# Kernel optimization log

Hardware: AMD Instinct MI355X
Metric: run time of the kernel (lower is better)

Reference implementation:

```python
import jax, jax.numpy as jnp
import numpy as np

# Faithful JAX reference for MVLiftingModule.lift_2D_to_3D with lifting_method='mean'.
# Torch semantics: for each batch, view, and part p in [1, parts_nb[b]] (in order),
# scatter-write the (weighted softmax) pixel prediction into each point that any
# Since each pixel's predicted part is unique (argmax), the winning pixel per point
# is the one maximizing key = pred_class * H*W + flat_pixel_index. We compute that
# deterministically via scatter-max, then gather features and voint-mean over views.

def setup_inputs() -> dict:
    key = jax.random.key(0)
    k1, k2, k3, k4, k5 = jax.random.split(key, 5)
    B, N, V, C, H, W = 4, 2048, 12, 50, 128, 128
    points = jax.random.normal(k1, (B, N, 3), dtype=jnp.float32)
    predictions_2d = jax.random.normal(k2, (B, V, C, H, W), dtype=jnp.float32)
    # -1 marks background pixels (no point), as in pytorch3d pix_to_face
    rendered_pix_to_point = jax.random.randint(k3, (B, V, 1, H, W), -1, N, dtype=jnp.int32)
    views_weights = jax.random.uniform(k4, (B, V, 1, 1, 1), dtype=jnp.float32)
    parts_nb = jax.random.randint(k5, (B,), 1, 7, dtype=jnp.int32)
    return {"points": points, "predictions_2d": predictions_2d,
            "rendered_pix_to_point": rendered_pix_to_point,
            "views_weights": views_weights, "parts_nb": parts_nb}


def reference(points, predictions_2d, rendered_pix_to_point, views_weights, parts_nb):
    B, N, _ = points.shape
    _, V, C, H, W = predictions_2d.shape
    P = H * W

    p2p = rendered_pix_to_point[:, :, 0]            # (B,V,H,W)
    valid = p2p != -1                                # pix_to_face_mask
    idx = jnp.where(valid, p2p % N, 0)               # invalid pixels -> point 0 (as in torch)

    probs = jax.nn.softmax(predictions_2d, axis=2)   # softmax over classes
    pred_max = jnp.argmax(probs, axis=2).astype(jnp.int32)   # (B,V,H,W)
    feats = (views_weights * probs).reshape(B, V, C, P)       # weighted predictions

    # pixel participates iff valid and its predicted part in [1, parts_nb[b]]
    mask_pix = valid & (pred_max >= 1) & (pred_max <= parts_nb[:, None, None, None])
    mask_pix = mask_pix.reshape(B, V, P)
    idx_f = idx.reshape(B, V, P)

    pix = jnp.arange(P, dtype=jnp.int32)
    kkey = pred_max.reshape(B, V, P) * P + pix
    kkey = jnp.where(mask_pix, kkey, -1)

    bi = jnp.arange(B)[:, None, None]
    vi = jnp.arange(V)[None, :, None]
    winner = jnp.full((B, V, N), -1, dtype=jnp.int32).at[bi, vi, idx_f].max(kkey)

    voints_mask = (winner >= 0)                      # (B,V,N)
    win_pix = jnp.where(voints_mask, winner % P, 0)  # winning pixel per point/view

    # gather weighted features at winning pixel: (B,V,C,N)
    point_feats = jnp.take_along_axis(feats, win_pix[:, :, None, :], axis=3)
    m = voints_mask.astype(feats.dtype)
    masked = point_feats * m[:, :, None, :]

    # vointmean: masked mean over views -> (B,C,N)
    denom = jnp.maximum(m.sum(axis=1), 1.0)          # (B,N)
    labels_3d_feats = masked.sum(axis=1) / denom[:, None, :]
    return labels_3d_feats
```

## Files before the change

### kernel.cpp

```cpp
#include <hip/hip_runtime.h>

#define B 4
#define N 2048
#define V 12
#define C 50
#define P 16384

__global__ __launch_bounds__(256) void k1_argmax_scatter(
    const float4* __restrict__ predv,
    const int4*  __restrict__ p2pv,
    const int*   __restrict__ parts_nb,
    int*         __restrict__ winner,
    float4*      __restrict__ sexp) {
  const int PQ = P / 4;
  int t = blockIdx.x * 256 + threadIdx.x;
  if (t >= B * V * PQ) return;
  int q  = t % PQ;
  int bv = t / PQ;
  int b  = bv / V;

  size_t base = (size_t)bv * C * PQ + q;
  float4 x = predv[base];
  float m0 = x.x, m1 = x.y, m2 = x.z, m3 = x.w;
  float s0 = __expf(x.x), s1 = __expf(x.y), s2 = __expf(x.z), s3 = __expf(x.w);
  int   a0 = 0,  a1 = 0,  a2 = 0,  a3 = 0;
  for (int c = 1; c < C; ++c) {
    float4 y = predv[base + (size_t)c * PQ];
    if (y.x > m0) { m0 = y.x; a0 = c; }
    if (y.y > m1) { m1 = y.y; a1 = c; }
    if (y.z > m2) { m2 = y.z; a2 = c; }
    if (y.w > m3) { m3 = y.w; a3 = c; }
    s0 += __expf(y.x); s1 += __expf(y.y);
    s2 += __expf(y.z); s3 += __expf(y.w);
  }
  sexp[(size_t)bv * PQ + q] = make_float4(s0, s1, s2, s3);

  int4 pt = p2pv[(size_t)bv * PQ + q];
  int pn = parts_nb[b];
  int p0 = q * 4;
  int* wbase = winner + bv * N;
  if (pt.x != -1 && a0 >= 1 && a0 <= pn) atomicMax(wbase + pt.x, a0 * P + p0);
  if (pt.y != -1 && a1 >= 1 && a1 <= pn) atomicMax(wbase + pt.y, a1 * P + p0 + 1);
  if (pt.z != -1 && a2 >= 1 && a2 <= pn) atomicMax(wbase + pt.z, a2 * P + p0 + 2);
  if (pt.w != -1 && a3 >= 1 && a3 <= pn) atomicMax(wbase + pt.w, a3 * P + p0 + 3);
}

__global__ __launch_bounds__(256) void k2_gather(
    const float* __restrict__ pred,
    const int*   __restrict__ winner,
    const float* __restrict__ sexp,
    const float* __restrict__ vw,
    float*       __restrict__ out) {
  int wid  = blockIdx.x * (256 / 64) + (threadIdx.x >> 6);
  int lane = threadIdx.x & 63;
  int b = wid >> 11;
  int n = wid & (N - 1);

  int wv[V];
  #pragma unroll
  for (int v = 0; v < V; ++v) wv[v] = winner[(b * V + v) * N + n];

  float acc = 0.f;
  int cnt = 0;
  #pragma unroll
  for (int v = 0; v < V; ++v) {
    bool valid = wv[v] >= 0;
    int wp = valid ? (wv[v] & (P - 1)) : 0;
    size_t bvo = (size_t)(b * V + v);
    float l = (lane < C) ? pred[(bvo * C + lane) * P + wp] : 0.f;
    float s = sexp[bvo * P + wp];
    float w = vw[b * V + v] / s;
    cnt += valid ? 1 : 0;
    acc += valid ? __expf(l) * w : 0.f;
  }
  float denom = (float)(cnt > 0 ? cnt : 1);
  if (lane < C)
    out[((size_t)b * C + lane) * N + n] = acc / denom;
}

extern "C" void kernel_launch(void* const* d_in, const int* in_sizes, int n_in,
                              void* d_out, int out_size, void* d_ws, size_t ws_size,
                              hipStream_t stream) {
  const float* pred  = (const float*)d_in[1];
  const int*   p2p   = (const int*)d_in[2];
  const float* vw    = (const float*)d_in[3];
  const int*   parts = (const int*)d_in[4];
  float* out = (float*)d_out;

  int*   winner = (int*)d_ws;
  float* sexp   = (float*)((char*)d_ws + (size_t)B * V * N * sizeof(int));

  hipMemsetAsync(winner, 0xFF, (size_t)B * V * N * sizeof(int), stream);

  int nthreads1 = B * V * (P / 4);
  k1_argmax_scatter<<<(nthreads1 + 255) / 256, 256, 0, stream>>>(
      (const float4*)pred, (const int4*)p2p, parts, winner, (float4*)sexp);

  k2_gather<<<(B * N) / 4, 256, 0, stream>>>(pred, winner, sexp, vw, out);
}
```

Before: 270.3 us.

## Compute softmax only for winning pixels and stage features in point-major buffer

Removes the per-pixel exp-sum from the argmax/scatter pass so that pass only computes argmax. A new extract kernel finds each point's winning pixel, computes its softmax and view weighting, and writes all classes contiguously into a per-point buffer. The final reduction then reads coalesced rows instead of strided gathers from the prediction tensor. This adds a kernel launch and a second read of the prediction tensor for winning pixels, which are scattered reads with a strided per-class pattern.

```diff
diff --git a/kernel.cpp b/kernel.cpp
--- a/kernel.cpp
+++ b/kernel.cpp
@@ -5,13 +5,13 @@
 #define V 12
 #define C 50
 #define P 16384
+#define CP 64
 
 __global__ __launch_bounds__(256) void k1_argmax_scatter(
     const float4* __restrict__ predv,
     const int4*  __restrict__ p2pv,
     const int*   __restrict__ parts_nb,
-    int*         __restrict__ winner,
-    float4*      __restrict__ sexp) {
+    int*         __restrict__ winner) {
   const int PQ = P / 4;
   int t = blockIdx.x * 256 + threadIdx.x;
   if (t >= B * V * PQ) return;
@@ -22,7 +22,6 @@
   size_t base = (size_t)bv * C * PQ + q;
   float4 x = predv[base];
   float m0 = x.x, m1 = x.y, m2 = x.z, m3 = x.w;
-  float s0 = __expf(x.x), s1 = __expf(x.y), s2 = __expf(x.z), s3 = __expf(x.w);
   int   a0 = 0,  a1 = 0,  a2 = 0,  a3 = 0;
   for (int c = 1; c < C; ++c) {
     float4 y = predv[base + (size_t)c * PQ];
@@ -30,10 +29,7 @@
     if (y.y > m1) { m1 = y.y; a1 = c; }
     if (y.z > m2) { m2 = y.z; a2 = c; }
     if (y.w > m3) { m3 = y.w; a3 = c; }
-    s0 += __expf(y.x); s1 += __expf(y.y);
-    s2 += __expf(y.z); s3 += __expf(y.w);
   }
-  sexp[(size_t)bv * PQ + q] = make_float4(s0, s1, s2, s3);
 
   int4 pt = p2pv[(size_t)bv * PQ + q];
   int pn = parts_nb[b];
@@ -45,37 +41,61 @@
   if (pt.w != -1 && a3 >= 1 && a3 <= pn) atomicMax(wbase + pt.w, a3 * P + p0 + 3);
 }
 
-__global__ __launch_bounds__(256) void k2_gather(
+__global__ __launch_bounds__(256) void k1b_extract(
     const float* __restrict__ pred,
+    const int*   __restrict__ p2p,
     const int*   __restrict__ winner,
-    const float* __restrict__ sexp,
     const float* __restrict__ vw,
+    float*       __restrict__ wfeat) {
+  int t = blockIdx.x * 256 + threadIdx.x;
+  int p  = t & (P - 1);
+  int bv = t >> 14;
+
+  int pt = p2p[(size_t)bv * P + p];
+  if (pt == -1) return;
+  int bvn = bv * N + pt;
+  int key = winner[bvn];
+  if (key < 0 || (key & (P - 1)) != p) return;
+
+  const float* pp = pred + (size_t)bv * C * P + p;
+  float e[C];
+  float s = 0.f;
+  #pragma unroll
+  for (int c = 0; c < C; ++c) e[c] = pp[(size_t)c * P];
+  #pragma unroll
+  for (int c = 0; c < C; ++c) { e[c] = __expf(e[c]); s += e[c]; }
+  float w = vw[bv] / s;
+
+  float4* dst = (float4*)(wfeat + (size_t)bvn * CP);
+  #pragma unroll
+  for (int c4 = 0; c4 < C / 4; ++c4) {
+    dst[c4] = make_float4(e[4*c4] * w, e[4*c4+1] * w, e[4*c4+2] * w, e[4*c4+3] * w);
+  }
+  wfeat[(size_t)bvn * CP + 48] = e[48] * w;
+  wfeat[(size_t)bvn * CP + 49] = e[49] * w;
+}
+
+__global__ __launch_bounds__(256) void k3_reduce(
+    const int*   __restrict__ winner,
+    const float* __restrict__ wfeat,
     float*       __restrict__ out) {
-  int wid  = blockIdx.x * (256 / 64) + (threadIdx.x >> 6);
+  int wid  = blockIdx.x * 4 + (threadIdx.x >> 6);
   int lane = threadIdx.x & 63;
   int b = wid >> 11;
   int n = wid & (N - 1);
-
-  int wv[V];
-  #pragma unroll
-  for (int v = 0; v < V; ++v) wv[v] = winner[(b * V + v) * N + n];
 
   float acc = 0.f;
   int cnt = 0;
   #pragma unroll
   for (int v = 0; v < V; ++v) {
-    bool valid = wv[v] >= 0;
-    int wp = valid ? (wv[v] & (P - 1)) : 0;
-    size_t bvo = (size_t)(b * V + v);
-    float l = (lane < C) ? pred[(bvo * C + lane) * P + wp] : 0.f;
-    float s = sexp[bvo * P + wp];
-    float w = vw[b * V + v] / s;
+    int bvn = (b * V + v) * N + n;
+    bool valid = winner[bvn] >= 0;
+    float f = (valid && lane < C) ? wfeat[(size_t)bvn * CP + lane] : 0.f;
     cnt += valid ? 1 : 0;
-    acc += valid ? __expf(l) * w : 0.f;
+    acc += f;
   }
-  float denom = (float)(cnt > 0 ? cnt : 1);
   if (lane < C)
-    out[((size_t)b * C + lane) * N + n] = acc / denom;
+    out[((size_t)b * C + lane) * N + n] = acc / (float)(cnt > 0 ? cnt : 1);
 }
 
 extern "C" void kernel_launch(void* const* d_in, const int* in_sizes, int n_in,
@@ -88,13 +108,17 @@
   float* out = (float*)d_out;
 
   int*   winner = (int*)d_ws;
-  float* sexp   = (float*)((char*)d_ws + (size_t)B * V * N * sizeof(int));
+  float* wfeat  = (float*)((char*)d_ws + (size_t)B * V * N * sizeof(int));
 
   hipMemsetAsync(winner, 0xFF, (size_t)B * V * N * sizeof(int), stream);
 
   int nthreads1 = B * V * (P / 4);
   k1_argmax_scatter<<<(nthreads1 + 255) / 256, 256, 0, stream>>>(
-      (const float4*)pred, (const int4*)p2p, parts, winner, (float4*)sexp);
+      (const float4*)pred, (const int4*)p2p, parts, winner);
 
-  k2_gather<<<(B * N) / 4, 256, 0, stream>>>(pred, winner, sexp, vw, out);
+  int nthreads1b = B * V * P;
+  k1b_extract<<<nthreads1b / 256, 256, 0, stream>>>(
+      pred, p2p, winner, vw, wfeat);
+
+  k3_reduce<<<(B * N) / 4, 256, 0, stream>>>(winner, wfeat, out);
 }
```

After: 259.8 us. -3.9%, faster.

## Compact winning-candidate softmax rows into a pool to avoid scattered prediction gathers

Applied to the files above, without the earlier changes.

Each pixel that passes the part mask now takes a slot from a global atomic counter. It writes its 50 exponentiated logits plus their sum into a compact pool row. A 64-bit key holding (class*P+pixel, slot) goes into the winner atomicMax. The reduce kernel then reads contiguous pool rows instead of gathering strided values from the full prediction tensor. This also skips the exp over all pixels in the first pass and drops the separate exp-sum buffer. The costs are a single contended global counter, uncoalesced per-thread pool writes, and 100 logits held in registers per thread.

```diff
diff --git a/kernel.cpp b/kernel.cpp
--- a/kernel.cpp
+++ b/kernel.cpp
@@ -5,77 +5,94 @@
 #define V 12
 #define C 50
 #define P 16384
+#define PH (P/2)
+#define PSTRIDE 56
 
-__global__ __launch_bounds__(256) void k1_argmax_scatter(
-    const float4* __restrict__ predv,
-    const int4*  __restrict__ p2pv,
+typedef unsigned long long u64;
+
+__global__ __launch_bounds__(256) void k1_fused(
+    const float2* __restrict__ predv,
+    const int2*  __restrict__ p2pv,
     const int*   __restrict__ parts_nb,
-    int*         __restrict__ winner,
-    float4*      __restrict__ sexp) {
-  const int PQ = P / 4;
+    u64*         __restrict__ winner,
+    unsigned int* __restrict__ counter,
+    float*       __restrict__ pool) {
   int t = blockIdx.x * 256 + threadIdx.x;
-  if (t >= B * V * PQ) return;
-  int q  = t % PQ;
-  int bv = t / PQ;
+  int q  = t & (PH - 1);
+  int bv = t >> 13;
   int b  = bv / V;
 
-  size_t base = (size_t)bv * C * PQ + q;
-  float4 x = predv[base];
-  float m0 = x.x, m1 = x.y, m2 = x.z, m3 = x.w;
-  float s0 = __expf(x.x), s1 = __expf(x.y), s2 = __expf(x.z), s3 = __expf(x.w);
-  int   a0 = 0,  a1 = 0,  a2 = 0,  a3 = 0;
+  size_t base = (size_t)bv * C * PH + q;
+  float l0[C], l1[C];
+  float m0, m1;
+  int a0 = 0, a1 = 0;
+  {
+    float2 x = predv[base];
+    l0[0] = x.x; l1[0] = x.y; m0 = x.x; m1 = x.y;
+  }
+  #pragma unroll
   for (int c = 1; c < C; ++c) {
-    float4 y = predv[base + (size_t)c * PQ];
+    float2 y = predv[base + (size_t)c * PH];
+    l0[c] = y.x; l1[c] = y.y;
     if (y.x > m0) { m0 = y.x; a0 = c; }
     if (y.y > m1) { m1 = y.y; a1 = c; }
-    if (y.z > m2) { m2 = y.z; a2 = c; }
-    if (y.w > m3) { m3 = y.w; a3 = c; }
-    s0 += __expf(y.x); s1 += __expf(y.y);
-    s2 += __expf(y.z); s3 += __expf(y.w);
   }
-  sexp[(size_t)bv * PQ + q] = make_float4(s0, s1, s2, s3);
 
-  int4 pt = p2pv[(size_t)bv * PQ + q];
+  int2 pt = p2pv[(size_t)bv * PH + q];
   int pn = parts_nb[b];
-  int p0 = q * 4;
-  int* wbase = winner + bv * N;
-  if (pt.x != -1 && a0 >= 1 && a0 <= pn) atomicMax(wbase + pt.x, a0 * P + p0);
-  if (pt.y != -1 && a1 >= 1 && a1 <= pn) atomicMax(wbase + pt.y, a1 * P + p0 + 1);
-  if (pt.z != -1 && a2 >= 1 && a2 <= pn) atomicMax(wbase + pt.z, a2 * P + p0 + 2);
-  if (pt.w != -1 && a3 >= 1 && a3 <= pn) atomicMax(wbase + pt.w, a3 * P + p0 + 3);
+  int p0 = q * 2;
+
+  bool v0 = (pt.x != -1) && (a0 >= 1) && (a0 <= pn);
+  bool v1 = (pt.y != -1) && (a1 >= 1) && (a1 <= pn);
+
+  if (v0) {
+    unsigned int slot = atomicAdd(counter, 1u);
+    u64 key = ((u64)(a0 * P + p0) << 20) | (u64)slot;
+    atomicMax(&winner[bv * N + pt.x], key);
+    float s = 0.f;
+    float* dst = pool + (size_t)slot * PSTRIDE;
+    #pragma unroll
+    for (int c = 0; c < C; ++c) { float e = __expf(l0[c]); dst[c] = e; s += e; }
+    dst[C] = s;
+  }
+  if (v1) {
+    unsigned int slot = atomicAdd(counter, 1u);
+    u64 key = ((u64)(a1 * P + p0 + 1) << 20) | (u64)slot;
+    atomicMax(&winner[bv * N + pt.y], key);
+    float s = 0.f;
+    float* dst = pool + (size_t)slot * PSTRIDE;
+    #pragma unroll
+    for (int c = 0; c < C; ++c) { float e = __expf(l1[c]); dst[c] = e; s += e; }
+    dst[C] = s;
+  }
 }
 
-__global__ __launch_bounds__(256) void k2_gather(
-    const float* __restrict__ pred,
-    const int*   __restrict__ winner,
-    const float* __restrict__ sexp,
+__global__ __launch_bounds__(256) void k3_reduce(
+    const u64*  __restrict__ winner,
+    const float* __restrict__ pool,
     const float* __restrict__ vw,
     float*       __restrict__ out) {
-  int wid  = blockIdx.x * (256 / 64) + (threadIdx.x >> 6);
+  int wid  = blockIdx.x * 4 + (threadIdx.x >> 6);
   int lane = threadIdx.x & 63;
   int b = wid >> 11;
   int n = wid & (N - 1);
-
-  int wv[V];
-  #pragma unroll
-  for (int v = 0; v < V; ++v) wv[v] = winner[(b * V + v) * N + n];
 
   float acc = 0.f;
   int cnt = 0;
   #pragma unroll
   for (int v = 0; v < V; ++v) {
-    bool valid = wv[v] >= 0;
-    int wp = valid ? (wv[v] & (P - 1)) : 0;
-    size_t bvo = (size_t)(b * V + v);
-    float l = (lane < C) ? pred[(bvo * C + lane) * P + wp] : 0.f;
-    float s = sexp[bvo * P + wp];
-    float w = vw[b * V + v] / s;
+    u64 key = winner[(b * V + v) * N + n];
+    bool valid = key != 0ull;
+    unsigned int slot = (unsigned int)(key & 0xFFFFFu);
+    const float* src = pool + (size_t)slot * PSTRIDE;
+    float e = (valid && lane < C) ? src[lane] : 0.f;
+    float s = valid ? src[C] : 1.f;
+    float f = valid ? (vw[b * V + v] / s) : 0.f;
     cnt += valid ? 1 : 0;
-    acc += valid ? __expf(l) * w : 0.f;
+    acc += e * f;
   }
-  float denom = (float)(cnt > 0 ? cnt : 1);
   if (lane < C)
-    out[((size_t)b * C + lane) * N + n] = acc / denom;
+    out[((size_t)b * C + lane) * N + n] = acc / (float)(cnt > 0 ? cnt : 1);
 }
 
 extern "C" void kernel_launch(void* const* d_in, const int* in_sizes, int n_in,
@@ -87,14 +104,16 @@
   const int*   parts = (const int*)d_in[4];
   float* out = (float*)d_out;
 
-  int*   winner = (int*)d_ws;
-  float* sexp   = (float*)((char*)d_ws + (size_t)B * V * N * sizeof(int));
+  char* ws = (char*)d_ws;
+  unsigned int* counter = (unsigned int*)ws;
+  u64*   winner = (u64*)(ws + 256);
+  float* pool   = (float*)(ws + 256 + (size_t)B * V * N * sizeof(u64));
 
-  hipMemsetAsync(winner, 0xFF, (size_t)B * V * N * sizeof(int), stream);
+  hipMemsetAsync(ws, 0, 256 + (size_t)B * V * N * sizeof(u64), stream);
 
-  int nthreads1 = B * V * (P / 4);
-  k1_argmax_scatter<<<(nthreads1 + 255) / 256, 256, 0, stream>>>(
-      (const float4*)pred, (const int4*)p2p, parts, winner, (float4*)sexp);
+  int nthreads = B * V * PH;
+  k1_fused<<<nthreads / 256, 256, 0, stream>>>(
+      (const float2*)pred, (const int2*)p2p, parts, winner, counter, pool);
 
-  k2_gather<<<(B * N) / 4, 256, 0, stream>>>(pred, winner, sexp, vw, out);
+  k3_reduce<<<(B * N) / 4, 256, 0, stream>>>(winner, pool, vw, out);
 }
```

After: 332.5 us. +23.0%, slower.
